# Kernel tuning notes

Hardware: AMD Instinct MI355X
Metric: run time of the kernel (lower is better)

The kernel has to match this reference:

```python
import jax, jax.numpy as jnp
import numpy as np

B, T, EMB, HEAD = 8, 2048, 1024, 1024

def setup_inputs() -> dict:
    key = jax.random.key(0)
    k1, k2, k3, k4 = jax.random.split(key, 4)
    s = 1.0 / np.sqrt(EMB)
    return {
        "x": jax.random.normal(k1, (B, T, EMB), dtype=jnp.float32),
        "Wq": jax.random.normal(k2, (HEAD, EMB), dtype=jnp.float32) * s,
        "Wk": jax.random.normal(k3, (HEAD, EMB), dtype=jnp.float32) * s,
        "Wv": jax.random.normal(k4, (HEAD, EMB), dtype=jnp.float32) * s,
    }

def reference(x, Wq, Wk, Wv):
    # Bias-free projections; torch Linear weight is [out, in] -> contract on last dim.
    q = jnp.einsum('btc,hc->bth', x, Wq)  # [B,T,HEAD]
    k = jnp.einsum('btc,hc->bth', x, Wk)
    v = jnp.einsum('btc,hc->bth', x, Wv)
    C = x.shape[-1]
    scale = jnp.asarray(C, x.dtype) ** -0.5  # NOTE: scales by emb dim C, as in source
    wei = jnp.einsum('bth,bsh->bts', q, k) * scale  # [B,T,T]
    Tn = x.shape[1]
    causal = jnp.tril(jnp.ones((Tn, Tn), dtype=bool))
    wei = jnp.where(causal, wei, -jnp.inf)
    wei = jax.nn.softmax(wei, axis=-1)
    # dropout omitted (eval mode / deterministic reference)
    out = jnp.einsum('bts,bsh->bth', wei, v)  # [B,T,HEAD]
    return out
```

## Files before the change

### kernel.cpp

```cpp
#include <hip/hip_runtime.h>

typedef unsigned short u16;
typedef short short8 __attribute__((ext_vector_type(8)));
typedef float f32x4 __attribute__((ext_vector_type(4)));

#define WS_K_OFF    33554432ULL
#define WS_PTRI     67108864ULL
#define WS_PART     104857600ULL
#define WS_NEED     105447424ULL

__device__ __forceinline__ u16 f2bf(float f) {
    union { float f; unsigned u; } c; c.f = f;
    unsigned r = c.u + 0x7fffu + ((c.u >> 16) & 1u);
    return (u16)(r >> 16);
}
__device__ __forceinline__ float bf2f(u16 h) {
    union { unsigned u; float f; } c; c.u = ((unsigned)h) << 16; return c.f;
}
__device__ __forceinline__ void gll16(const u16* g, u16* l) {
    __builtin_amdgcn_global_load_lds(
        (const __attribute__((address_space(1))) void*)g,
        (__attribute__((address_space(3))) void*)l, 16, 0, 0);
}

template<int AMODE>
__device__ __forceinline__ void gemm_pipe(
    const u16* __restrict__ A, int lda,
    const u16* __restrict__ B, int ldb,
    int m0, int n0, int nk, u16* lds, f32x4 acc[8][4])
{
    const int tid  = threadIdx.x;
    const int lane = tid & 63;
    const int w    = tid >> 6;
    const int wm   = w >> 2, wn = w & 3;
    const int kg   = lane >> 4, l15 = lane & 15;
    const int r0   = w * 32 + (lane >> 2);
    const int s0   = (lane & 3) ^ ((r0 >> 1) & 3);

    const int ldA = AMODE ? 256 : lda;
    const u16* Ar0 = A + (size_t)(m0 + r0) * ldA + s0 * 8;
    const u16* Ar1 = Ar0 + 16 * ldA;
    const u16* Br0 = B + (size_t)(n0 + r0) * ldb + s0 * 8;
    const u16* Br1 = Br0 + 16 * ldb;

    auto aoff = [&](int t) -> int {
        return AMODE ? ((t >> 3) * 65536 + (t & 7) * 32) : t * 32;
    };
    auto STAGE = [&](int t) {
        const int ao = aoff(t), bo = t * 32, buf = (t & 3) * 16384;
        u16* dA = lds + buf + w * 1024;
        u16* dB = lds + buf + 8192 + w * 1024;
        gll16(Ar0 + ao, dA);
        gll16(Ar1 + ao, dA + 512);
        gll16(Br0 + bo, dB);
        gll16(Br1 + bo, dB + 512);
    };
    auto LDA8 = [&](short8* fa, int t) {
        const u16* h = lds + (t & 3) * 16384 + wm * 4096;
        #pragma unroll
        for (int mt = 0; mt < 8; ++mt) {
            const int row = mt * 16 + l15;
            fa[mt] = *reinterpret_cast<const short8*>(
                h + row * 32 + ((kg ^ ((row >> 1) & 3)) << 3));
        }
    };
    auto LDB4 = [&](short8* fb, int t) {
        const u16* h = lds + (t & 3) * 16384 + 8192 + wn * 2048;
        #pragma unroll
        for (int nt = 0; nt < 4; ++nt) {
            const int row = nt * 16 + l15;
            fb[nt] = *reinterpret_cast<const short8*>(
                h + row * 32 + ((kg ^ ((row >> 1) & 3)) << 3));
        }
    };
    auto MFMA32 = [&](short8* fa, short8* fb) {
        __builtin_amdgcn_s_setprio(1);
        #pragma unroll
        for (int mt = 0; mt < 8; ++mt)
            #pragma unroll
            for (int nt = 0; nt < 4; ++nt)
                acc[mt][nt] = __builtin_amdgcn_mfma_f32_16x16x32_bf16(
                    fa[mt], fb[nt], acc[mt][nt], 0, 0, 0);
        __builtin_amdgcn_s_setprio(0);
    };

    STAGE(0); STAGE(1); STAGE(2);
    asm volatile("s_waitcnt vmcnt(4)" ::: "memory");
    __builtin_amdgcn_s_barrier();

    short8 faA[8], faB[8], fb[4];
    LDA8(faA, 0);

    for (int t = 0; t < nk; t += 2) {
        LDB4(fb, t);
        LDA8(faB, t + 1);
        if (t + 3 < nk) STAGE(t + 3);
        MFMA32(faA, fb);
        if (t + 3 < nk) asm volatile("s_waitcnt vmcnt(4)" ::: "memory");
        else            asm volatile("s_waitcnt vmcnt(0)" ::: "memory");
        __builtin_amdgcn_s_barrier();

        LDB4(fb, t + 1);
        if (t + 2 < nk) LDA8(faA, t + 2);
        if (t + 4 < nk) STAGE(t + 4);
        MFMA32(faB, fb);
        if (t + 4 < nk) asm volatile("s_waitcnt vmcnt(4)" ::: "memory");
        else            asm volatile("s_waitcnt vmcnt(0)" ::: "memory");
        __builtin_amdgcn_s_barrier();
    }
}

__global__ __launch_bounds__(256) void cvt_bf16(
    const float* __restrict__ x,
    const float* __restrict__ Wq,
    const float* __restrict__ Wk,
    const float* __restrict__ Wv,
    u16* __restrict__ dst)
{
    const size_t e = ((size_t)blockIdx.x * 256 + threadIdx.x) * 8;
    const float* src;
    if (e < (size_t)16777216) {
        src = x + e;
    } else {
        size_t j = e - 16777216;
        int z = (int)(j >> 20);
        const float* Wz = (z == 0) ? Wq : (z == 1) ? Wk : Wv;
        src = Wz + (j & 1048575);
    }
    float4 a = *reinterpret_cast<const float4*>(src);
    float4 b = *reinterpret_cast<const float4*>(src + 4);
    short8 v;
    v[0] = (short)f2bf(a.x); v[1] = (short)f2bf(a.y);
    v[2] = (short)f2bf(a.z); v[3] = (short)f2bf(a.w);
    v[4] = (short)f2bf(b.x); v[5] = (short)f2bf(b.y);
    v[6] = (short)f2bf(b.z); v[7] = (short)f2bf(b.w);
    *reinterpret_cast<short8*>(dst + e) = v;
}

__global__ __launch_bounds__(512, 2) void qkv_pipe(
    const u16* __restrict__ xb, const u16* __restrict__ Wb,
    u16* __restrict__ Qo, u16* __restrict__ Ko, u16* __restrict__ VTo, int zbase)
{
    __shared__ u16 L[65536];
    const int tid = threadIdx.x, lane = tid & 63, w = tid >> 6;
    const int wm = w >> 2, wn = w & 3, kg = lane >> 4, l15 = lane & 15;
    const int m0 = blockIdx.x * 256, n0 = blockIdx.y * 256;
    const int z = blockIdx.z + zbase;

    const f32x4 z4 = {0.f, 0.f, 0.f, 0.f};
    f32x4 acc[8][4];
    #pragma unroll
    for (int i = 0; i < 8; ++i)
        #pragma unroll
        for (int j = 0; j < 4; ++j) acc[i][j] = z4;

    gemm_pipe<0>(xb, 1024, Wb + (size_t)z * 1048576, 1024, m0, n0, 32, L, acc);

    if (z < 2) {
        u16* O = (z == 0) ? Qo : Ko;
        #pragma unroll
        for (int mt = 0; mt < 8; ++mt) {
            const int row0 = m0 + wm * 128 + mt * 16 + kg * 4;
            #pragma unroll
            for (int nt = 0; nt < 4; ++nt) {
                const int col = n0 + wn * 64 + nt * 16 + l15;
                #pragma unroll
                for (int r = 0; r < 4; ++r)
                    O[(size_t)(row0 + r) * 1024 + col] = f2bf(acc[mt][nt][r]);
            }
        }
    } else {
        #pragma unroll
        for (int mt = 0; mt < 8; ++mt) {
            const int row0 = m0 + wm * 128 + mt * 16 + kg * 4;
            #pragma unroll
            for (int nt = 0; nt < 4; ++nt) {
                const int col = n0 + wn * 64 + nt * 16 + l15;
                #pragma unroll
                for (int r = 0; r < 4; ++r) {
                    const int rr = row0 + r;
                    VTo[((size_t)(rr >> 11) * 1024 + col) * 2048 + (rr & 2047)] = f2bf(acc[mt][nt][r]);
                }
            }
        }
    }
}

template<int AMODE>
__device__ __forceinline__ void gemm_tri128(
    const u16* __restrict__ A, int lda,
    const u16* __restrict__ B, int ldb, int nk, u16* L, f32x4 acc[4][4])
{
    const int tid = threadIdx.x, lane = tid & 63, w = tid >> 6;
    const int wm = w >> 1, wn = w & 1, kg = lane >> 4, l15 = lane & 15;

    const int rA = w * 32 + (lane >> 2);
    const int sA = (lane & 3) ^ ((rA >> 1) & 3);
    const int rB = w * 16 + (lane >> 2);
    const int sB = (lane & 3) ^ ((rB >> 1) & 3);
    const int ldA = AMODE ? 256 : lda;
    const u16* Ar0 = A + (size_t)rA * ldA + sA * 8;
    const u16* Ar1 = Ar0 + 16 * ldA;
    const u16* Br0 = B + (size_t)rB * ldb + sB * 8;

    auto aoff = [&](int t) -> int {
        return AMODE ? ((t >> 3) * 65536 + (t & 7) * 32) : t * 32;
    };
    auto STAGE = [&](int t) {
        u16* d = L + (t % 3) * 12288;
        gll16(Ar0 + aoff(t), d + w * 1024);
        gll16(Ar1 + aoff(t), d + w * 1024 + 512);
        gll16(Br0 + t * 32,  d + 8192 + w * 512);
    };
    auto LDA4 = [&](short8* fa, int t) {
        const u16* h = L + (t % 3) * 12288;
        #pragma unroll
        for (int mt = 0; mt < 4; ++mt) {
            const int row = wm * 64 + mt * 16 + l15;
            fa[mt] = *reinterpret_cast<const short8*>(
                h + row * 32 + ((kg ^ ((row >> 1) & 3)) << 3));
        }
    };
    auto LDB4 = [&](short8* fb, int t) {
        const u16* h = L + (t % 3) * 12288 + 8192;
        #pragma unroll
        for (int nt = 0; nt < 4; ++nt) {
            const int row = wn * 64 + nt * 16 + l15;
            fb[nt] = *reinterpret_cast<const short8*>(
                h + row * 32 + ((kg ^ ((row >> 1) & 3)) << 3));
        }
    };

    STAGE(0); STAGE(1);
    asm volatile("s_waitcnt vmcnt(3)" ::: "memory");
    __builtin_amdgcn_s_barrier();

    short8 fa[4], fb[4];
    for (int t = 0; t < nk; ++t) {
        LDA4(fa, t);
        LDB4(fb, t);
        if (t + 2 < nk) STAGE(t + 2);
        __builtin_amdgcn_s_setprio(1);
        #pragma unroll
        for (int mt = 0; mt < 4; ++mt)
            #pragma unroll
            for (int nt = 0; nt < 4; ++nt)
                acc[mt][nt] = __builtin_amdgcn_mfma_f32_16x16x32_bf16(
                    fa[mt], fb[nt], acc[mt][nt], 0, 0, 0);
        __builtin_amdgcn_s_setprio(0);
        if (t + 2 < nk) asm volatile("s_waitcnt vmcnt(3)" ::: "memory");
        else            asm volatile("s_waitcnt vmcnt(0)" ::: "memory");
        __builtin_amdgcn_s_barrier();
    }
}

__global__ __launch_bounds__(512, 4) void sp128(
    const u16* __restrict__ Q, const u16* __restrict__ K,
    u16* __restrict__ Ptri, float* __restrict__ part)
{
    __shared__ u16 L[36864];
    int jj = blockIdx.x;
    const int b = jj / 72;
    int r = jj - b * 72;
    int qb = 0;
    while (r >= 2 * qb + 2) { r -= 2 * qb + 2; ++qb; }
    const int kb = r;

    const int tid = threadIdx.x, lane = tid & 63, w = tid >> 6;
    const int wm = w >> 1, wn = w & 1, kg = lane >> 4, l15 = lane & 15;

    const f32x4 z4 = {0.f, 0.f, 0.f, 0.f};
    f32x4 acc[4][4];
    #pragma unroll
    for (int a_ = 0; a_ < 4; ++a_)
        #pragma unroll
        for (int j = 0; j < 4; ++j) acc[a_][j] = z4;

    gemm_tri128<0>(Q + (size_t)(b * 2048 + qb * 256) * 1024, 1024,
                   K + (size_t)(b * 2048 + kb * 128) * 1024, 1024,
                   32, L, acc);

    u16* Pt = Ptri + ((size_t)b * 36 + (qb * (qb + 1)) / 2 + (kb >> 1)) * 65536
                   + (kb & 1) * 128;
    float* psum = (float*)L;
    #pragma unroll
    for (int mt = 0; mt < 4; ++mt) {
        #pragma unroll
        for (int rr = 0; rr < 4; ++rr) {
            const int lt = wm * 64 + mt * 16 + kg * 4 + rr;
            const int gt = qb * 256 + lt;
            float ps = 0.f;
            #pragma unroll
            for (int nt = 0; nt < 4; ++nt) {
                const int lcol = wn * 64 + nt * 16 + l15;
                const int gs = kb * 128 + lcol;
                const float p = (gs <= gt) ? __expf(acc[mt][nt][rr] * 0.03125f) : 0.f;
                ps += p;
                Pt[(size_t)lt * 256 + lcol] = f2bf(p);
            }
            #pragma unroll
            for (int d = 1; d < 16; d <<= 1) ps += __shfl_xor(ps, d, 64);
            if (l15 == 0) psum[lt * 2 + wn] = ps;
        }
    }
    __syncthreads();
    if (tid < 256) {
        const float s = psum[tid * 2] + psum[tid * 2 + 1];
        part[(size_t)b * 18432 + (qb * qb + qb) * 256 + tid * (2 * qb + 2) + kb] = s;
    }
}

__global__ __launch_bounds__(512, 2) void sp_old(
    const u16* __restrict__ Q, const u16* __restrict__ K, u16* __restrict__ P)
{
    const int qb = blockIdx.x, kb = blockIdx.y, b = blockIdx.z;
    if (kb > qb) return;
    __shared__ u16 L[65536];
    const int tid = threadIdx.x, lane = tid & 63, w = tid >> 6;
    const int wm = w >> 2, wn = w & 3, kg = lane >> 4, l15 = lane & 15;

    const f32x4 z4 = {0.f, 0.f, 0.f, 0.f};
    f32x4 acc[8][4];
    #pragma unroll
    for (int i = 0; i < 8; ++i)
        #pragma unroll
        for (int j = 0; j < 4; ++j) acc[i][j] = z4;

    gemm_pipe<0>(Q, 1024, K, 1024, b * 2048 + qb * 256, b * 2048 + kb * 256, 32, L, acc);

    u16* Pb = P + (size_t)b * 2048 * 2048;
    #pragma unroll
    for (int mt = 0; mt < 8; ++mt) {
        const int trow0 = qb * 256 + wm * 128 + mt * 16 + kg * 4;
        #pragma unroll
        for (int nt = 0; nt < 4; ++nt) {
            const int scol = kb * 256 + wn * 64 + nt * 16 + l15;
            #pragma unroll
            for (int r = 0; r < 4; ++r) {
                const int trow = trow0 + r;
                const float p = (scol <= trow) ? __expf(acc[mt][nt][r] * 0.03125f) : 0.f;
                Pb[(size_t)trow * 2048 + scol] = f2bf(p);
            }
        }
    }
}

__global__ __launch_bounds__(512, 4) void pv128(
    const u16* __restrict__ Ptri, const u16* __restrict__ VT,
    const float* __restrict__ part, float* __restrict__ out)
{
    __shared__ u16 L[36864];
    const int i = blockIdx.x;
    const int c = i >> 7;
    const int j = (i >> 1) & 63;
    const int s = i & 1;
    const int q  = s ? c : 7 - c;
    const int b  = j >> 3;
    const int nb = j & 7;
    const int nk = (q + 1) * 8;

    const int tid = threadIdx.x, lane = tid & 63, w = tid >> 6;
    const int wm = w >> 1, wn = w & 1, kg = lane >> 4, l15 = lane & 15;

    const f32x4 z4 = {0.f, 0.f, 0.f, 0.f};
    f32x4 acc[4][4];
    #pragma unroll
    for (int a_ = 0; a_ < 4; ++a_)
        #pragma unroll
        for (int jx = 0; jx < 4; ++jx) acc[a_][jx] = z4;

    gemm_tri128<1>(Ptri + ((size_t)b * 36 + (q * (q + 1)) / 2) * 65536, 256,
                   VT + ((size_t)b * 1024 + nb * 128) * 2048, 2048,
                   nk, L, acc);

    float* Lf = (float*)L;
    if (tid < 256) {
        const int nkb = 2 * q + 2;
        const float* pp = part + (size_t)b * 18432 + (q * q + q) * 256 + tid * nkb;
        float sum = 0.f;
        for (int kb = 0; kb < nkb; ++kb) sum += pp[kb];
        Lf[tid] = 1.f / sum;
    }
    __syncthreads();

    #pragma unroll
    for (int mt = 0; mt < 4; ++mt) {
        const int lt0 = wm * 64 + mt * 16 + kg * 4;
        const size_t grow0 = (size_t)b * 2048 + q * 256 + lt0;
        float rs[4];
        #pragma unroll
        for (int r = 0; r < 4; ++r) rs[r] = Lf[lt0 + r];
        #pragma unroll
        for (int nt = 0; nt < 4; ++nt) {
            const int col = nb * 128 + wn * 64 + nt * 16 + l15;
            #pragma unroll
            for (int r = 0; r < 4; ++r)
                out[(grow0 + r) * 1024 + col] = acc[mt][nt][r] * rs[r];
        }
    }
}

__global__ __launch_bounds__(512, 2) void pv_old(
    const u16* __restrict__ P, const u16* __restrict__ VT, float* __restrict__ Of)
{
    const int b = blockIdx.x >> 3, qblk = blockIdx.x & 7;
    const int nb = blockIdx.y;
    const int nk = (qblk + 1) * 8;
    __shared__ u16 L[65536];
    const int tid = threadIdx.x, lane = tid & 63, w = tid >> 6;
    const int wm = w >> 2, wn = w & 3, kg = lane >> 4, l15 = lane & 15;

    const f32x4 z4 = {0.f, 0.f, 0.f, 0.f};
    f32x4 acc[8][4];
    #pragma unroll
    for (int i = 0; i < 8; ++i)
        #pragma unroll
        for (int j = 0; j < 4; ++j) acc[i][j] = z4;

    gemm_pipe<0>(P + (size_t)b * 2048 * 2048, 2048,
                 VT + (size_t)b * 1024 * 2048, 2048,
                 qblk * 256, nb * 256, nk, L, acc);

    #pragma unroll
    for (int mt = 0; mt < 8; ++mt) {
        const int trow0 = qblk * 256 + wm * 128 + mt * 16 + kg * 4;
        #pragma unroll
        for (int nt = 0; nt < 4; ++nt) {
            const int col = nb * 256 + wn * 64 + nt * 16 + l15;
            #pragma unroll
            for (int r = 0; r < 4; ++r)
                Of[((size_t)b * 2048 + trow0 + r) * 1024 + col] = acc[mt][nt][r];
        }
    }
}

__global__ __launch_bounds__(256) void finalize(
    const u16* __restrict__ P, const float* __restrict__ Of, float* __restrict__ out)
{
    const int row = blockIdx.x;
    const int tid = threadIdx.x;
    const int b = row >> 11, t = row & 2047;
    const int len = ((t >> 8) + 1) * 256;
    const u16* prow = P + ((size_t)b * 2048 + t) * 2048;

    float s = 0.f;
    const int i = tid * 8;
    if (i < len) {
        short8 v = *reinterpret_cast<const short8*>(prow + i);
        #pragma unroll
        for (int j = 0; j < 8; ++j) s += bf2f((u16)v[j]);
    }
    #pragma unroll
    for (int d = 1; d < 64; d <<= 1) s += __shfl_xor(s, d, 64);

    __shared__ float red[4];
    if ((tid & 63) == 0) red[tid >> 6] = s;
    __syncthreads();
    const float rinv = 1.f / (red[0] + red[1] + red[2] + red[3]);

    const size_t o = (size_t)row * 1024 + tid * 4;
    f32x4 v = *reinterpret_cast<const f32x4*>(Of + o);
    v[0] *= rinv; v[1] *= rinv; v[2] *= rinv; v[3] *= rinv;
    *reinterpret_cast<f32x4*>(out + o) = v;
}

extern "C" void kernel_launch(void* const* d_in, const int* in_sizes, int n_in,
                              void* d_out, int out_size, void* d_ws, size_t ws_size,
                              hipStream_t stream) {
    const float* x  = (const float*)d_in[0];
    const float* Wq = (const float*)d_in[1];
    const float* Wk = (const float*)d_in[2];
    const float* Wv = (const float*)d_in[3];

    u16* xb = (u16*)d_out;
    u16* Wb = xb + (size_t)16777216;

    cvt_bf16<<<dim3(9728), 256, 0, stream>>>(x, Wq, Wk, Wv, xb);

    if (ws_size >= WS_NEED) {
        u16*   Qb   = (u16*)d_ws;
        u16*   Kb   = (u16*)((char*)d_ws + WS_K_OFF);
        u16*   Pt   = (u16*)((char*)d_ws + WS_PTRI);
        float* part = (float*)((char*)d_ws + WS_PART);
        u16*   VTb  = Qb;

        qkv_pipe<<<dim3(64, 4, 2), 512, 0, stream>>>(xb, Wb, Qb, Kb, Qb, 0);
        sp128<<<dim3(576), 512, 0, stream>>>(Qb, Kb, Pt, part);
        qkv_pipe<<<dim3(64, 4, 1), 512, 0, stream>>>(xb, Wb, Qb, Kb, VTb, 2);
        pv128<<<dim3(512), 512, 0, stream>>>(Pt, VTb, part, (float*)d_out);
    } else {
        u16* Qb  = (u16*)d_ws;
        u16* Kb  = Qb + (size_t)16384 * 1024;
        u16* VTb = Kb + (size_t)16384 * 1024;
        float* Of = (float*)d_ws;
        u16* Pb = (u16*)d_out;

        qkv_pipe<<<dim3(64, 4, 3), 512, 0, stream>>>(xb, Wb, Qb, Kb, VTb, 0);
        sp_old<<<dim3(8, 8, 8), 512, 0, stream>>>(Qb, Kb, Pb);
        pv_old<<<dim3(64, 4), 512, 0, stream>>>(Pb, VTb, Of);
        finalize<<<dim3(16384), 256, 0, stream>>>(Pb, Of, (float*)d_out);
    }
}
```

Measured before the change: 260.4 us.

## Split GEMM mainloop into two half-tile phases with separate A/B staging

Restructures the bf16 GEMM mainloop. Each k-step now runs in two phases, each doing 4x4 MFMAs on half of the A rows. The global-to-LDS loads for A and B are issued in separate phases, and barriers plus explicit lgkmcnt waits are placed between them. This halves the A fragment registers, which may reduce register pressure, and spreads memory issue more finely across the compute. In exchange it drops the previous cross-iteration LDS prefetch of A fragments and adds more barriers per k-step, which can expose LDS latency.

After: 266.3 us. 1.02x slower.

```diff
diff --git a/kernel.cpp b/kernel.cpp
--- a/kernel.cpp
+++ b/kernel.cpp
@@ -46,21 +46,22 @@
     auto aoff = [&](int t) -> int {
         return AMODE ? ((t >> 3) * 65536 + (t & 7) * 32) : t * 32;
     };
-    auto STAGE = [&](int t) {
-        const int ao = aoff(t), bo = t * 32, buf = (t & 3) * 16384;
-        u16* dA = lds + buf + w * 1024;
-        u16* dB = lds + buf + 8192 + w * 1024;
-        gll16(Ar0 + ao, dA);
-        gll16(Ar1 + ao, dA + 512);
-        gll16(Br0 + bo, dB);
-        gll16(Br1 + bo, dB + 512);
-    };
-    auto LDA8 = [&](short8* fa, int t) {
+    auto STAGE_A = [&](int t) {
+        u16* dA = lds + (t & 3) * 16384 + w * 1024;
+        gll16(Ar0 + aoff(t), dA);
+        gll16(Ar1 + aoff(t), dA + 512);
+    };
+    auto STAGE_B = [&](int t) {
+        u16* dB = lds + (t & 3) * 16384 + 8192 + w * 1024;
+        gll16(Br0 + t * 32, dB);
+        gll16(Br1 + t * 32, dB + 512);
+    };
+    auto LDA4 = [&](short8* fa, int t, int mb) {
         const u16* h = lds + (t & 3) * 16384 + wm * 4096;
         #pragma unroll
-        for (int mt = 0; mt < 8; ++mt) {
-            const int row = mt * 16 + l15;
-            fa[mt] = *reinterpret_cast<const short8*>(
+        for (int mi = 0; mi < 4; ++mi) {
+            const int row = (mb + mi) * 16 + l15;
+            fa[mi] = *reinterpret_cast<const short8*>(
                 h + row * 32 + ((kg ^ ((row >> 1) & 3)) << 3));
         }
     };
@@ -73,39 +74,45 @@
                 h + row * 32 + ((kg ^ ((row >> 1) & 3)) << 3));
         }
     };
-    auto MFMA32 = [&](short8* fa, short8* fb) {
+
+    STAGE_A(0); STAGE_B(0);
+    STAGE_A(1); STAGE_B(1);
+    STAGE_A(2); STAGE_B(2);
+    asm volatile("s_waitcnt vmcnt(8)" ::: "memory");
+    __builtin_amdgcn_s_barrier();
+
+    short8 fa[4], fb[4];
+    for (int t = 0; t < nk; ++t) {
+        LDB4(fb, t);
+        LDA4(fa, t, 0);
+        if (t + 3 < nk) STAGE_A(t + 3);
+        __builtin_amdgcn_s_barrier();
+        asm volatile("s_waitcnt lgkmcnt(0)" ::: "memory");
         __builtin_amdgcn_s_setprio(1);
         #pragma unroll
-        for (int mt = 0; mt < 8; ++mt)
+        for (int mi = 0; mi < 4; ++mi)
             #pragma unroll
             for (int nt = 0; nt < 4; ++nt)
-                acc[mt][nt] = __builtin_amdgcn_mfma_f32_16x16x32_bf16(
-                    fa[mt], fb[nt], acc[mt][nt], 0, 0, 0);
+                acc[mi][nt] = __builtin_amdgcn_mfma_f32_16x16x32_bf16(
+                    fa[mi], fb[nt], acc[mi][nt], 0, 0, 0);
         __builtin_amdgcn_s_setprio(0);
-    };
-
-    STAGE(0); STAGE(1); STAGE(2);
-    asm volatile("s_waitcnt vmcnt(4)" ::: "memory");
-    __builtin_amdgcn_s_barrier();
-
-    short8 faA[8], faB[8], fb[4];
-    LDA8(faA, 0);
-
-    for (int t = 0; t < nk; t += 2) {
-        LDB4(fb, t);
-        LDA8(faB, t + 1);
-        if (t + 3 < nk) STAGE(t + 3);
-        MFMA32(faA, fb);
-        if (t + 3 < nk) asm volatile("s_waitcnt vmcnt(4)" ::: "memory");
-        else            asm volatile("s_waitcnt vmcnt(0)" ::: "memory");
         __builtin_amdgcn_s_barrier();
 
-        LDB4(fb, t + 1);
-        if (t + 2 < nk) LDA8(faA, t + 2);
-        if (t + 4 < nk) STAGE(t + 4);
-        MFMA32(faB, fb);
-        if (t + 4 < nk) asm volatile("s_waitcnt vmcnt(4)" ::: "memory");
-        else            asm volatile("s_waitcnt vmcnt(0)" ::: "memory");
+        LDA4(fa, t, 4);
+        if (t + 3 < nk) STAGE_B(t + 3);
+        __builtin_amdgcn_s_barrier();
+        asm volatile("s_waitcnt lgkmcnt(0)" ::: "memory");
+        __builtin_amdgcn_s_setprio(1);
+        #pragma unroll
+        for (int mi = 0; mi < 4; ++mi)
+            #pragma unroll
+            for (int nt = 0; nt < 4; ++nt)
+                acc[4 + mi][nt] = __builtin_amdgcn_mfma_f32_16x16x32_bf16(
+                    fa[mi], fb[nt], acc[4 + mi][nt], 0, 0, 0);
+        __builtin_amdgcn_s_setprio(0);
+        if (t + 3 < nk)      asm volatile("s_waitcnt vmcnt(8)" ::: "memory");
+        else if (t + 2 < nk) asm volatile("s_waitcnt vmcnt(4)" ::: "memory");
+        else                 asm volatile("s_waitcnt vmcnt(0)" ::: "memory");
         __builtin_amdgcn_s_barrier();
     }
 }
```

## Stage V-transpose through LDS and fuse QKV projections when workspace allows

Applied to the files above, without the earlier changes.

The V projection epilogue now packs four bf16 values per lane into LDS, then writes the transposed V^T in 16-byte contiguous rows to global memory instead of scattered 2-byte strided stores. A new larger-workspace path keeps Q, K and V^T in separate buffers, so all three projections run in one launch instead of two separate qkv_pipe launches around the score kernel. This aims to cut uncoalesced write traffic and one launch. The cost is extra LDS use and two barriers in the epilogue, plus a larger workspace requirement; if the workspace is too small, the old path runs.

Measured after the change: 254.6 us. 1.02x faster.

```diff
diff --git a/kernel.cpp b/kernel.cpp
--- a/kernel.cpp
+++ b/kernel.cpp
@@ -3,11 +3,17 @@
 typedef unsigned short u16;
 typedef short short8 __attribute__((ext_vector_type(8)));
 typedef float f32x4 __attribute__((ext_vector_type(4)));
+typedef unsigned long long u64;
 
 #define WS_K_OFF    33554432ULL
 #define WS_PTRI     67108864ULL
 #define WS_PART     104857600ULL
 #define WS_NEED     105447424ULL
+#define W2_K        33554432ULL
+#define W2_VT       67108864ULL
+#define W2_PTRI     100663296ULL
+#define W2_PART     138412032ULL
+#define W2_NEED     139001856ULL
 
 __device__ __forceinline__ u16 f2bf(float f) {
     union { float f; unsigned u; } c; c.f = f;
@@ -170,18 +176,37 @@
             }
         }
     } else {
-        #pragma unroll
-        for (int mt = 0; mt < 8; ++mt) {
-            const int row0 = m0 + wm * 128 + mt * 16 + kg * 4;
-            #pragma unroll
-            for (int nt = 0; nt < 4; ++nt) {
-                const int col = n0 + wn * 64 + nt * 16 + l15;
+        const int b    = m0 >> 11;
+        const int mloc = m0 & 2047;
+        const int t8   = (tid & 31) * 8;
+        const int hh   = tid >> 5;
+        #pragma unroll
+        for (int half = 0; half < 2; ++half) {
+            if ((wn >> 1) == half) {
+                const int hb = (wn & 1) * 64;
                 #pragma unroll
-                for (int r = 0; r < 4; ++r) {
-                    const int rr = row0 + r;
-                    VTo[((size_t)(rr >> 11) * 1024 + col) * 2048 + (rr & 2047)] = f2bf(acc[mt][nt][r]);
+                for (int mt = 0; mt < 8; ++mt) {
+                    const int tl = wm * 128 + mt * 16 + kg * 4;
+                    #pragma unroll
+                    for (int nt = 0; nt < 4; ++nt) {
+                        const int hl = hb + nt * 16 + l15;
+                        u64 pk = (u64)f2bf(acc[mt][nt][0])
+                               | ((u64)f2bf(acc[mt][nt][1]) << 16)
+                               | ((u64)f2bf(acc[mt][nt][2]) << 32)
+                               | ((u64)f2bf(acc[mt][nt][3]) << 48);
+                        *reinterpret_cast<u64*>(&L[hl * 264 + tl]) = pk;
+                    }
                 }
             }
+            __syncthreads();
+            #pragma unroll
+            for (int p = 0; p < 8; ++p) {
+                const int hl = p * 16 + hh;
+                short8 v = *reinterpret_cast<const short8*>(&L[hl * 264 + t8]);
+                *reinterpret_cast<short8*>(
+                    &VTo[((size_t)b * 1024 + n0 + half * 128 + hl) * 2048 + mloc + t8]) = v;
+            }
+            __syncthreads();
         }
     }
 }
@@ -477,7 +502,17 @@
 
     cvt_bf16<<<dim3(9728), 256, 0, stream>>>(x, Wq, Wk, Wv, xb);
 
-    if (ws_size >= WS_NEED) {
+    if (ws_size >= W2_NEED) {
+        u16*   Qb   = (u16*)d_ws;
+        u16*   Kb   = (u16*)((char*)d_ws + W2_K);
+        u16*   VTb  = (u16*)((char*)d_ws + W2_VT);
+        u16*   Pt   = (u16*)((char*)d_ws + W2_PTRI);
+        float* part = (float*)((char*)d_ws + W2_PART);
+
+        qkv_pipe<<<dim3(64, 4, 3), 512, 0, stream>>>(xb, Wb, Qb, Kb, VTb, 0);
+        sp128<<<dim3(576), 512, 0, stream>>>(Qb, Kb, Pt, part);
+        pv128<<<dim3(512), 512, 0, stream>>>(Pt, VTb, part, (float*)d_out);
+    } else if (ws_size >= WS_NEED) {
         u16*   Qb   = (u16*)d_ws;
         u16*   Kb   = (u16*)((char*)d_ws + WS_K_OFF);
         u16*   Pt   = (u16*)((char*)d_ws + WS_PTRI);
```
